# Kernel optimization log

Measured on AMD Instinct MI355X. Metric: run time of the kernel, lower is better.

Reference implementation:

```python
import jax, jax.numpy as jnp
import numpy as np

B, G, D, H, W = 2, 8, 32, 128, 160
NEIGH = 9           # evaluate_neighbors
PROP = 1            # propagation_out_range - 1
PAD1 = int(np.sqrt(NEIGH) / 2) + PROP      # = 2
PAD2 = PAD1 * 2                            # = 4


def setup_inputs() -> dict:
    key = jax.random.key(0)
    ks = jax.random.split(key, 8)
    x1 = jax.random.normal(ks[0], (B, G, D, H, W), jnp.float32)
    offset = jax.random.uniform(ks[1], (B, 2 * NEIGH, H, W), jnp.float32)
    weight = jax.random.uniform(ks[2], (B, 1, H, W), jnp.float32)
    # 1x1x1 Conv3d weights stored as [out_ch, in_ch]; BN folded to scale/bias (eval mode)
    w0 = jax.random.normal(ks[3], (16, G), jnp.float32) * 0.1
    bn0_scale = jnp.ones((16,), jnp.float32)
    bn0_bias = jnp.zeros((16,), jnp.float32)
    w1 = jax.random.normal(ks[4], (8, 16), jnp.float32) * 0.1
    bn1_scale = jnp.ones((8,), jnp.float32)
    bn1_bias = jnp.zeros((8,), jnp.float32)
    w_sim = jax.random.normal(ks[5], (1, 8), jnp.float32) * 0.1
    b_sim = jnp.zeros((1,), jnp.float32)
    return {"x1": x1, "offset": offset, "weight": weight,
            "w0": w0, "bn0_scale": bn0_scale, "bn0_bias": bn0_bias,
            "w1": w1, "bn1_scale": bn1_scale, "bn1_bias": bn1_bias,
            "w_sim": w_sim, "b_sim": b_sim}


def _conv1x1_bn_relu(x, w, scale, bias):
    # x: [B,Cin,D,H,W], w: [Cout,Cin]
    y = jnp.einsum('bcdhw,oc->bodhw', x, w)
    return jax.nn.relu(y * scale[None, :, None, None, None] + bias[None, :, None, None, None])


def reference(x1, offset, weight, w0, bn0_scale, bn0_bias, w1, bn1_scale, bn1_bias, w_sim, b_sim):
    h = _conv1x1_bn_relu(x1, w0, bn0_scale, bn0_bias)          # [B,16,D,H,W]
    h = _conv1x1_bn_relu(h, w1, bn1_scale, bn1_bias)            # [B,8,D,H,W]
    sim = jnp.einsum('bcdhw,oc->bodhw', h, w_sim) + b_sim[None, :, None, None, None]
    sim = sim[:, 0]                                             # [B,D,H,W]
    b, d, hgt, wid = sim.shape
    p1 = jnp.pad(sim, ((0, 0), (0, 0), (PAD1, PAD1), (PAD1, PAD1)), mode='reflect')
    p2 = jnp.pad(sim, ((0, 0), (0, 0), (PAD2, PAD2), (PAD2, PAD2)), mode='reflect')
    side = int(np.sqrt(NEIGH))  # 3
    acc = jnp.zeros_like(sim)
    for s in range(NEIGH):
        iy, ix = s // side, s % side
        # wide-dilation crop (stride (PROP+1)*2 = 4) over the double-padded map
        c2 = p2[:, :, iy * 4: iy * 4 + hgt, ix * 4: ix * 4 + wid]
        # narrow-dilation crop (stride PROP+1 = 2) over the single-padded map
        c1 = p1[:, :, iy * 2: iy * 2 + hgt, ix * 2: ix * 2 + wid]
        w_wide = offset[:, s][:, None]            # [B,1,H,W] -> broadcast over depth
        w_narrow = offset[:, s + NEIGH][:, None]
        acc = acc + (w_narrow * c1 + w_wide * c2) * 0.5
    return acc * weight                                          # weight [B,1,H,W]
```

## Files before the change

kernel.cpp:

```cpp
#include <hip/hip_runtime.h>

#define Bc 2
#define Gc 8
#define Dc 32
#define Hc 128
#define Wc 160
#define HW (Hc * Wc)
#define DHW (Dc * HW)

#define TH 32
#define TW 40
#define R  4
#define SH (TH + 2 * R)
#define SW (TW + 2 * R)
#define SIMN (SH * SW)
#define NQ (SIMN / 4)
#define QPR (SW / 4)

__global__ __launch_bounds__(512)
void fused_kernel(
    const float* __restrict__ x1, const float* __restrict__ offset,
    const float* __restrict__ weight,
    const float* __restrict__ w0, const float* __restrict__ s0, const float* __restrict__ b0,
    const float* __restrict__ w1, const float* __restrict__ s1, const float* __restrict__ b1,
    const float* __restrict__ wsim, const float* __restrict__ bsim,
    float* __restrict__ out)
{
    __shared__ __align__(16) float sms[SIMN];
    __shared__ float smw[289];
    const int tid = threadIdx.x;

    if (tid < 289) {
        const int i = tid;
        float v;
        if (i < 128)      v = w0[i] * s0[i >> 3];
        else if (i < 144) v = b0[i - 128];
        else if (i < 272) v = w1[i - 144] * s1[(i - 144) >> 4];
        else if (i < 280) v = b1[i - 272];
        else if (i < 288) v = wsim[i - 280];
        else              v = bsim[0];
        smw[i] = v;
    }

    const int blk = blockIdx.x;
    const int d   = blk & 31;
    const int t   = (blk >> 5) & 15;
    const int b   = blk >> 9;
    const int h0t = (t >> 2) * TH;
    const int w0t = (t & 3) * TW;

    __syncthreads();

    const float* sw0 = smw;
    const float* sb0 = smw + 128;
    const float* sw1 = smw + 144;
    const float* sb1 = smw + 272;
    const float* sws = smw + 280;
    const float  sbs = smw[288];

    const float* xb = x1 + (size_t)b * (Gc * DHW) + (size_t)d * HW;

    if (tid < NQ) {
        const int q   = tid;
        const int ty  = q / QPR;
        const int tx0 = (q - ty * QPR) * 4;
        int gh = h0t - R + ty;
        gh = gh < 0 ? -gh : (gh >= Hc ? 2 * Hc - 2 - gh : gh);
        const int gw0 = w0t - R + tx0;

        float4 xv[Gc];
        if (gw0 >= 0 && gw0 <= Wc - 4) {
            const float* p = xb + gh * Wc + gw0;
#pragma unroll
            for (int g = 0; g < Gc; ++g)
                xv[g] = *reinterpret_cast<const float4*>(p + g * DHW);
        } else {
            int gw[4];
#pragma unroll
            for (int j = 0; j < 4; ++j) {
                int x = gw0 + j;
                gw[j] = x < 0 ? -x : (x >= Wc ? 2 * Wc - 2 - x : x);
            }
            const float* p = xb + gh * Wc;
#pragma unroll
            for (int g = 0; g < Gc; ++g) {
                xv[g].x = p[g * DHW + gw[0]];
                xv[g].y = p[g * DHW + gw[1]];
                xv[g].z = p[g * DHW + gw[2]];
                xv[g].w = p[g * DHW + gw[3]];
            }
        }

        float4 acc1[8];
#pragma unroll
        for (int c = 0; c < 8; ++c) {
            const float bb = sb1[c];
            acc1[c].x = bb; acc1[c].y = bb; acc1[c].z = bb; acc1[c].w = bb;
        }

#pragma unroll
        for (int o = 0; o < 16; ++o) {
            float ax = sb0[o], ay = ax, az = ax, aw = ax;
#pragma unroll
            for (int g = 0; g < Gc; ++g) {
                const float wv = sw0[o * Gc + g];
                ax = fmaf(wv, xv[g].x, ax);
                ay = fmaf(wv, xv[g].y, ay);
                az = fmaf(wv, xv[g].z, az);
                aw = fmaf(wv, xv[g].w, aw);
            }
            ax = fmaxf(ax, 0.f);
            ay = fmaxf(ay, 0.f);
            az = fmaxf(az, 0.f);
            aw = fmaxf(aw, 0.f);
#pragma unroll
            for (int c = 0; c < 8; ++c) {
                const float wv = sw1[c * 16 + o];
                acc1[c].x = fmaf(wv, ax, acc1[c].x);
                acc1[c].y = fmaf(wv, ay, acc1[c].y);
                acc1[c].z = fmaf(wv, az, acc1[c].z);
                acc1[c].w = fmaf(wv, aw, acc1[c].w);
            }
        }

        float sx = sbs, sy = sbs, sz = sbs, sw = sbs;
#pragma unroll
        for (int c = 0; c < 8; ++c) {
            const float ws = sws[c];
            sx = fmaf(ws, fmaxf(acc1[c].x, 0.f), sx);
            sy = fmaf(ws, fmaxf(acc1[c].y, 0.f), sy);
            sz = fmaf(ws, fmaxf(acc1[c].z, 0.f), sz);
            sw = fmaf(ws, fmaxf(acc1[c].w, 0.f), sw);
        }

        float4 r; r.x = sx; r.y = sy; r.z = sz; r.w = sw;
        *reinterpret_cast<float4*>(&sms[q * 4]) = r;
    }

    __syncthreads();

    const float* offb = offset + (size_t)b * 18 * HW;
    const float* wtb  = weight + (size_t)b * HW;
    float* outb = out + (size_t)(b * Dc + d) * HW;

#pragma unroll 1
    for (int k = 0; k < 3; ++k) {
        const int idx = k * 512 + tid;
        if (idx < TH * TW) {
            const int oy  = idx / TW;
            const int ox  = idx - oy * TW;
            const int hw  = (h0t + oy) * Wc + (w0t + ox);

            float off[18];
#pragma unroll
            for (int s = 0; s < 18; ++s)
                off[s] = offb[s * HW + hw];
            const float wt = wtb[hw] * 0.5f;

            const float* sp = sms + (oy + R) * SW + (ox + R);
            float a = 0.f;
#pragma unroll
            for (int s = 0; s < 9; ++s) {
                const int dy = s / 3 - 1, dx = s % 3 - 1;
                a = fmaf(off[s + 9], sp[(dy * 2) * SW + dx * 2],
                    fmaf(off[s],     sp[(dy * 4) * SW + dx * 4], a));
            }
            outb[hw] = a * wt;
        }
    }
}

extern "C" void kernel_launch(void* const* d_in, const int* in_sizes, int n_in,
                              void* d_out, int out_size, void* d_ws, size_t ws_size,
                              hipStream_t stream)
{
    const float* x1     = (const float*)d_in[0];
    const float* offset = (const float*)d_in[1];
    const float* weight = (const float*)d_in[2];
    const float* w0     = (const float*)d_in[3];
    const float* s0     = (const float*)d_in[4];
    const float* b0     = (const float*)d_in[5];
    const float* w1     = (const float*)d_in[6];
    const float* s1     = (const float*)d_in[7];
    const float* b1     = (const float*)d_in[8];
    const float* wsim   = (const float*)d_in[9];
    const float* bsim   = (const float*)d_in[10];
    float* out = (float*)d_out;

    fused_kernel<<<1024, 512, 0, stream>>>(x1, offset, weight,
                                           w0, s0, b0, w1, s1, b1, wsim, bsim,
                                           out);
}
```

Baseline: 122.0 us.

## Vectorize stencil phase with float4 loads and prefetch offsets before barrier

The stencil phase now has each thread handle four adjacent output pixels, using float4 global loads for the offset and weight maps, float4/float2 shared-memory reads, and a single float4 store. The offset and weight loads are issued before the __syncthreads, behind a sched_barrier, so their latency overlaps the convolution phase and barrier wait. This replaces a three-iteration scalar loop, but keeps 18 float4 offsets (72 registers) live across the barrier, raising register pressure at 512 threads per block.

```diff
diff --git a/kernel.cpp b/kernel.cpp
--- a/kernel.cpp
+++ b/kernel.cpp
@@ -16,6 +16,8 @@
 #define SIMN (SH * SW)
 #define NQ (SIMN / 4)
 #define QPR (SW / 4)
+#define NQ2 (TH * TW / 4)
+#define QPR2 (TW / 4)
 
 __global__ __launch_bounds__(512)
 void fused_kernel(
@@ -137,36 +139,48 @@
         *reinterpret_cast<float4*>(&sms[q * 4]) = r;
     }
 
+    __builtin_amdgcn_sched_barrier(0);
+
+    const int oy  = tid / QPR2;
+    const int ox  = (tid - oy * QPR2) * 4;
+    const int hw4 = (h0t + oy) * Wc + (w0t + ox);
+
+    float4 off4[18];
+    float4 wt4;
+    if (tid < NQ2) {
+        const float* offb = offset + (size_t)b * 18 * HW;
+#pragma unroll
+        for (int s = 0; s < 18; ++s)
+            off4[s] = *reinterpret_cast<const float4*>(offb + s * HW + hw4);
+        wt4 = *reinterpret_cast<const float4*>(weight + (size_t)b * HW + hw4);
+    }
+
     __syncthreads();
 
-    const float* offb = offset + (size_t)b * 18 * HW;
-    const float* wtb  = weight + (size_t)b * HW;
-    float* outb = out + (size_t)(b * Dc + d) * HW;
-
-#pragma unroll 1
-    for (int k = 0; k < 3; ++k) {
-        const int idx = k * 512 + tid;
-        if (idx < TH * TW) {
-            const int oy  = idx / TW;
-            const int ox  = idx - oy * TW;
-            const int hw  = (h0t + oy) * Wc + (w0t + ox);
-
-            float off[18];
-#pragma unroll
-            for (int s = 0; s < 18; ++s)
-                off[s] = offb[s * HW + hw];
-            const float wt = wtb[hw] * 0.5f;
-
-            const float* sp = sms + (oy + R) * SW + (ox + R);
-            float a = 0.f;
-#pragma unroll
-            for (int s = 0; s < 9; ++s) {
-                const int dy = s / 3 - 1, dx = s % 3 - 1;
-                a = fmaf(off[s + 9], sp[(dy * 2) * SW + dx * 2],
-                    fmaf(off[s],     sp[(dy * 4) * SW + dx * 4], a));
-            }
-            outb[hw] = a * wt;
-        }
+    if (tid < NQ2) {
+        const float* sp = sms + (oy + R) * SW + (ox + R);
+        float ax = 0.f, ay = 0.f, az = 0.f, aw = 0.f;
+#pragma unroll
+        for (int s = 0; s < 9; ++s) {
+            const int dy = s / 3 - 1, dx = s % 3 - 1;
+            const float4 cw = *reinterpret_cast<const float4*>(sp + dy * 4 * SW + dx * 4);
+            const float* np = sp + dy * 2 * SW + dx * 2;
+            const float2 n0 = *reinterpret_cast<const float2*>(np);
+            const float2 n1 = *reinterpret_cast<const float2*>(np + 2);
+            const float4 ow = off4[s];
+            const float4 on = off4[s + 9];
+            ax = fmaf(on.x, n0.x, fmaf(ow.x, cw.x, ax));
+            ay = fmaf(on.y, n0.y, fmaf(ow.y, cw.y, ay));
+            az = fmaf(on.z, n1.x, fmaf(ow.z, cw.z, az));
+            aw = fmaf(on.w, n1.y, fmaf(ow.w, cw.w, aw));
+        }
+        float4 r;
+        r.x = ax * 0.5f * wt4.x;
+        r.y = ay * 0.5f * wt4.y;
+        r.z = az * 0.5f * wt4.z;
+        r.w = aw * 0.5f * wt4.w;
+        float* outb = out + (size_t)(b * Dc + d) * HW;
+        *reinterpret_cast<float4*>(outb + hw4) = r;
     }
 }
 
```

After: 120.0 us. Within noise of the previous version (-1.6%).
